# Kernel optimization log

Measured on AMD Instinct MI355X. Metric: run time of the kernel, lower is better.

Reference implementation:

```python
import jax, jax.numpy as jnp
import numpy as np

TEMPERATURE = 0.5
NEG_INF = -1e30  # mask value for diagonal in logsumexp (exact -inf also fine)


def _l2norm(x, eps=1e-12):
    # matches F.normalize(dim=1)
    n = jnp.sqrt(jnp.sum(x * x, axis=1, keepdims=True))
    return x / jnp.maximum(n, eps)


def setup_inputs() -> dict:
    key = jax.random.key(0)
    k1, k2, k3 = jax.random.split(key, 3)
    B, D, Q = 2048, 512, 32768
    return {
        "z_i": jax.random.normal(k1, (B, D), dtype=jnp.float32),
        "z_j": jax.random.normal(k2, (B, D), dtype=jnp.float32),
        "queue": jax.random.normal(k3, (Q, D), dtype=jnp.float32),
    }


def reference(z_i, z_j, queue):
    z = jnp.concatenate([z_i, z_j], axis=0)          # [N, D]
    N = z.shape[0]
    features = _l2norm(z)                            # [N, D]
    queue_norm = _l2norm(queue)                      # [Q, D]

    # NN retrieval from the support set
    sims_q = jnp.matmul(features, queue_norm.T)      # [N, Q]
    nn_idx = jnp.argmax(sims_q, axis=1)              # [N]
    nn_feats = queue_norm[nn_idx]                    # [N, D]

    # contrastive similarity between NNs and features
    sim = jnp.matmul(nn_feats, features.T) / TEMPERATURE  # [N, N]

    # positives: off-diagonals at +/- N//2
    sim_i_j = jnp.diagonal(sim, offset=N // 2)       # [N/2]
    sim_j_i = jnp.diagonal(sim, offset=-(N // 2))    # [N/2]
    positive_samples = jnp.concatenate([sim_i_j, sim_j_i], axis=0)  # [N]

    # negatives: all off-diagonal entries per row -> logsumexp with diag masked
    diag_mask = jnp.eye(N, dtype=bool)
    sim_masked = jnp.where(diag_mask, NEG_INF, sim)
    repulsion = jnp.mean(jax.scipy.special.logsumexp(sim_masked, axis=1))

    attraction = -jnp.mean(positive_samples)
    return attraction + repulsion
```

## Files before the change

### kernel.cpp

```cpp
#include <hip/hip_runtime.h>
#include <cstdint>

#define NFEAT 4096
#define NHALF 2048
#define DDIM  512
#define QROWS 32768

typedef unsigned short u16;
typedef unsigned char  u8;
typedef unsigned int   u32;
typedef unsigned long long u64;

typedef float  f32x16_t __attribute__((ext_vector_type(16)));
typedef int    i32x4_t  __attribute__((ext_vector_type(4)));
typedef int    i32x8_t  __attribute__((ext_vector_type(8)));

typedef const __attribute__((address_space(1))) void* gas_ptr;
typedef __attribute__((address_space(3))) void* las_ptr;

__device__ __forceinline__ u32 fkey(float f) {
  u32 u = __float_as_uint(f);
  return (u & 0x80000000u) ? ~u : (u | 0x80000000u);
}

__global__ void k_norm(const float* __restrict__ zi, const float* __restrict__ zj,
                       const float* __restrict__ queue,
                       u8* __restrict__ feat8T, u8* __restrict__ queue8T) {
  int gw = (int)((blockIdx.x * blockDim.x + threadIdx.x) >> 6);
  int lane = threadIdx.x & 63;
  const float* src; u8* dstT; int r31;
  if (gw < NFEAT) {
    src = (gw < NHALF) ? (zi + (size_t)gw * DDIM) : (zj + (size_t)(gw - NHALF) * DDIM);
    dstT = feat8T + (size_t)(gw >> 5) * 16384; r31 = gw & 31;
  } else {
    int r = gw - NFEAT;
    src = queue + (size_t)r * DDIM;
    dstT = queue8T + (size_t)(r >> 5) * 16384; r31 = r & 31;
  }
  float4 v0 = reinterpret_cast<const float4*>(src)[lane * 2];
  float4 v1 = reinterpret_cast<const float4*>(src)[lane * 2 + 1];
  float ss = v0.x*v0.x + v0.y*v0.y + v0.z*v0.z + v0.w*v0.w
           + v1.x*v1.x + v1.y*v1.y + v1.z*v1.z + v1.w*v1.w;
  #pragma unroll
  for (int off = 32; off >= 1; off >>= 1) ss += __shfl_xor(ss, off);
  float inv = 1.0f / fmaxf(sqrtf(ss), 1e-12f);
  float n0 = v0.x*inv, n1 = v0.y*inv, n2 = v0.z*inv, n3 = v0.w*inv;
  float n4 = v1.x*inv, n5 = v1.y*inv, n6 = v1.z*inv, n7 = v1.w*inv;
  u32 p01, p23, p45, p67;
  asm("v_cvt_pk_fp8_f32 %0, %1, %2" : "=v"(p01) : "v"(n0), "v"(n1));
  asm("v_cvt_pk_fp8_f32 %0, %1, %2" : "=v"(p23) : "v"(n2), "v"(n3));
  asm("v_cvt_pk_fp8_f32 %0, %1, %2" : "=v"(p45) : "v"(n4), "v"(n5));
  asm("v_cvt_pk_fp8_f32 %0, %1, %2" : "=v"(p67) : "v"(n6), "v"(n7));
  uint2 w8;
  w8.x = (p01 & 0xFFFFu) | (p23 << 16);
  w8.y = (p45 & 0xFFFFu) | (p67 << 16);
  size_t toff = (size_t)(lane >> 3) * 2048 + ((lane >> 2) & 1) * 1024
              + ((lane >> 1) & 1) * 512 + r31 * 16 + (lane & 1) * 8;
  *reinterpret_cast<uint2*>(dstT + toff) = w8;
}

#define SB0() __builtin_amdgcn_sched_barrier(0)
#define LGKM0_SB() do { asm volatile("s_waitcnt lgkmcnt(0)" ::: "memory"); SB0(); } while (0)
#define VMCNT4() asm volatile("s_waitcnt vmcnt(4)" ::: "memory")
#define VMCNT0() asm volatile("s_waitcnt vmcnt(0)" ::: "memory")
#define SBAR() __builtin_amdgcn_s_barrier()
#define RD(dst, base, off) asm volatile("ds_read_b128 %0, %1 offset:" off \
                                        : "=v"(dst) : "v"(base))
#define MFMA8(ACC, AV, BV) \
  ACC = __builtin_amdgcn_mfma_scale_f32_32x32x64_f8f6f4(AV, BV, ACC, 0, 0, 0, \
        0x7F7F7F7F, 0, 0x7F7F7F7F)

__global__ __launch_bounds__(512, 3) void k_argmax_gemm8(
    const u8* __restrict__ feat8T, const u8* __restrict__ queue8T,
    u64* __restrict__ part) {
  __shared__ u8 lds[16384];
  const int tid = threadIdx.x;
  const int w = tid >> 6, lane = tid & 63;
  const int wr = w >> 2, wc = w & 3;
  const int l31 = lane & 31, hi = lane >> 5;
  const int bid = (int)blockIdx.x;
  const int wg = (bid & 7) * 512 + (bid >> 3);
  const int mt = wg >> 4, ft = wg & 15;
  const int brow = mt * 128, bcol = ft * 256;

  const u8* pA = queue8T + (size_t)((brow >> 5) + (tid >> 7)) * 16384 + (tid & 127) * 16;
  const u32 dA = (u32)(size_t)(las_ptr)&lds[tid * 16];

  const u32 aAd = (u32)(size_t)(las_ptr)&lds[wr * 4096 + hi * 1024 + l31 * 16];

  const u8* pB0 = feat8T + (size_t)((bcol >> 5) + wc * 2) * 16384 + hi * 1024 + l31 * 16;
  const u8* pB1 = pB0 + 16384;

  f32x16_t acc00 = {}, acc01 = {}, acc10 = {}, acc11 = {};

  auto stageA = [&](int b, int t) {
    __builtin_amdgcn_global_load_lds((gas_ptr)(pA + t * 2048),
        (las_ptr)(size_t)(dA + (u32)(b * 8192)), 16, 0, 0);
  };

  stageA(0, 0);
  VMCNT0();
  SBAR();

  #pragma unroll
  for (int t = 0; t < 8; t++) {
    const u8* q0 = pB0 + t * 2048;
    const u8* q1 = pB1 + t * 2048;
    i32x4_t b0l = *reinterpret_cast<const i32x4_t*>(q0);
    i32x4_t b0h = *reinterpret_cast<const i32x4_t*>(q0 + 512);
    i32x4_t b1l = *reinterpret_cast<const i32x4_t*>(q1);
    i32x4_t b1h = *reinterpret_cast<const i32x4_t*>(q1 + 512);
    if (t < 7) stageA((t + 1) & 1, t + 1);
    const u32 xa = aAd + (u32)((t & 1) * 8192);
    i32x4_t a0l, a0h, a1l, a1h;
    RD(a0l, xa, "0");    RD(a0h, xa, "512");
    RD(a1l, xa, "2048"); RD(a1h, xa, "2560");
    LGKM0_SB();
    i32x8_t A0 = __builtin_shufflevector(a0l, a0h, 0, 1, 2, 3, 4, 5, 6, 7);
    i32x8_t A1 = __builtin_shufflevector(a1l, a1h, 0, 1, 2, 3, 4, 5, 6, 7);
    i32x8_t B0 = __builtin_shufflevector(b0l, b0h, 0, 1, 2, 3, 4, 5, 6, 7);
    i32x8_t B1 = __builtin_shufflevector(b1l, b1h, 0, 1, 2, 3, 4, 5, 6, 7);
    __builtin_amdgcn_s_setprio(1);
    MFMA8(acc00, A0, B0); MFMA8(acc01, A0, B1);
    MFMA8(acc10, A1, B0); MFMA8(acc11, A1, B1);
    __builtin_amdgcn_s_setprio(0);
    if (t < 7) { VMCNT0(); SBAR(); }
  }

  const int mslot = mt * 2 + wr;
#define AMAX_N(ACC0, ACC1, NOFF) do { \
    float bv = -3.0e38f; int br = 0; \
    _Pragma("unroll") \
    for (int reg = 0; reg < 16; reg++) { \
      float v = ACC0[reg]; int lr = (reg & 3) + 8 * (reg >> 2); \
      if (v > bv) { bv = v; br = lr; } } \
    _Pragma("unroll") \
    for (int reg = 0; reg < 16; reg++) { \
      float v = ACC1[reg]; int lr = 32 + (reg & 3) + 8 * (reg >> 2); \
      if (v > bv) { bv = v; br = lr; } } \
    u32 q = (u32)(brow + wr * 64 + br + 4 * hi); \
    u64 key = ((u64)fkey(bv) << 32) | (u64)(0xFFFFFFFFu - q); \
    u64 o = __shfl_xor(key, 32); \
    key = key > o ? key : o; \
    int j = bcol + wc * 64 + NOFF + l31; \
    if (hi == 0) part[(size_t)j * 512 + mslot] = key; \
  } while (0)
  AMAX_N(acc00, acc10, 0);
  AMAX_N(acc01, acc11, 32);
#undef AMAX_N
}

__global__ void k_reduce_gather(const u64* __restrict__ part,
                                const u8* __restrict__ queue8T,
                                u8* __restrict__ nn8T) {
  int row = (int)((blockIdx.x * blockDim.x + threadIdx.x) >> 6);
  int lane = threadIdx.x & 63;
  const u64* p = part + (size_t)row * 512;
  u64 best = 0;
  #pragma unroll
  for (int i = 0; i < 8; i++) { u64 v = p[lane * 8 + i]; best = best > v ? best : v; }
  #pragma unroll
  for (int off = 1; off < 64; off <<= 1) { u64 o = __shfl_xor(best, off); best = best > o ? best : o; }
  int g = (int)(0xFFFFFFFFu - (u32)(best & 0xFFFFFFFFu));
  if (lane < 32) {
    const uint4 v = *reinterpret_cast<const uint4*>(
        queue8T + (size_t)(g >> 5) * 16384 + lane * 512 + (g & 31) * 16);
    *reinterpret_cast<uint4*>(
        nn8T + (size_t)(row >> 5) * 16384 + lane * 512 + (row & 31) * 16) = v;
  }
}

#define FP8_TILE(XA, XB) do { \
    i32x4_t a00, a01, a10, a11, b00, b01, b10, b11; \
    RD(a00, XA, "0"); RD(a01, XA, "512"); \
    RD(a10, XA, "2048"); RD(a11, XA, "2560"); \
    RD(b00, XB, "0"); RD(b01, XB, "512"); \
    RD(b10, XB, "2048"); RD(b11, XB, "2560"); \
    LGKM0_SB(); \
    i32x8_t A0 = __builtin_shufflevector(a00, a01, 0, 1, 2, 3, 4, 5, 6, 7); \
    i32x8_t A1 = __builtin_shufflevector(a10, a11, 0, 1, 2, 3, 4, 5, 6, 7); \
    i32x8_t B0 = __builtin_shufflevector(b00, b01, 0, 1, 2, 3, 4, 5, 6, 7); \
    i32x8_t B1 = __builtin_shufflevector(b10, b11, 0, 1, 2, 3, 4, 5, 6, 7); \
    __builtin_amdgcn_s_setprio(1); \
    MFMA8(acc00, A0, B0); \
    MFMA8(acc01, A0, B1); \
    MFMA8(acc10, A1, B0); \
    MFMA8(acc11, A1, B1); \
    __builtin_amdgcn_s_setprio(0); \
  } while (0)

#define FP8_MAIN_LOOP() do { \
  stage(0, 0); stage(1, 1); \
  VMCNT4(); \
  SBAR(); \
  _Pragma("unroll") \
  for (int t = 0; t < 8; t++) { \
    if (t <= 5) stage((t + 2) % 3, t + 2); \
    const u32 bb = (u32)((t % 3) * 16384); \
    FP8_TILE(aAd + bb, bAd + bb); \
    if (t < 7) { \
      if (t <= 5) VMCNT4(); else VMCNT0(); \
      SBAR(); \
    } \
  } } while (0)

__global__ __launch_bounds__(256, 2) void k_sim_gemm8(
    const u8* __restrict__ feat8T, const u8* __restrict__ nn8T,
    float2* __restrict__ lsep, float* __restrict__ pos) {
  __shared__ u8 lds[49152];
  const int tid = threadIdx.x;
  const int w = tid >> 6, lane = tid & 63;
  const int wr = w >> 1, wc = w & 1;
  const int l31 = lane & 31, hi = lane >> 5;
  const int bid = (int)blockIdx.x;
  const int wg = (bid & 7) * 128 + (bid >> 3);
  const int mt = wg >> 5, nt = wg & 31;
  const int mtb = mt * 128, ntb = nt * 128;

  const u8* pA = feat8T + (size_t)(mtb >> 5) * 16384 + (tid >> 7) * 16384 + (tid & 127) * 16;
  const u8* pB = nn8T   + (size_t)(ntb >> 5) * 16384 + (tid >> 7) * 16384 + (tid & 127) * 16;
  const u32 dA = (u32)(size_t)(las_ptr)&lds[tid * 16];
  const u32 dB = dA + 8192;

  const u32 aAd = (u32)(size_t)(las_ptr)&lds[wr * 4096 + hi * 1024 + l31 * 16];
  const u32 bAd = (u32)(size_t)(las_ptr)&lds[8192 + wc * 4096 + hi * 1024 + l31 * 16];

  f32x16_t acc00 = {}, acc01 = {}, acc10 = {}, acc11 = {};

  auto stage = [&](int b, int t) {
    const u32 base = (u32)(b * 16384);
    __builtin_amdgcn_global_load_lds((gas_ptr)(pA + t * 2048),         (las_ptr)(size_t)(dA + base), 16, 0, 0);
    __builtin_amdgcn_global_load_lds((gas_ptr)(pA + 32768 + t * 2048), (las_ptr)(size_t)(dA + base + 4096), 16, 0, 0);
    __builtin_amdgcn_global_load_lds((gas_ptr)(pB + t * 2048),         (las_ptr)(size_t)(dB + base), 16, 0, 0);
    __builtin_amdgcn_global_load_lds((gas_ptr)(pB + 32768 + t * 2048), (las_ptr)(size_t)(dB + base + 4096), 16, 0, 0);
  };

  FP8_MAIN_LOOP();

  const int mslot = mt * 2 + wr;
  const int ibase = mtb + wr * 64 + 4 * hi;
  #pragma unroll
  for (int n = 0; n < 2; n++) {
    const int j = ntb + wc * 64 + n * 32 + l31;
    const int jp = j ^ NHALF;
    float mx = -3.0e38f;
    #pragma unroll
    for (int m = 0; m < 2; m++) {
      #pragma unroll
      for (int reg = 0; reg < 16; reg++) {
        float v = (n == 0 ? (m == 0 ? acc00[reg] : acc10[reg])
                          : (m == 0 ? acc01[reg] : acc11[reg])) * 2.0f;
        int i = ibase + m * 32 + (reg & 3) + 8 * (reg >> 2);
        if (i == jp) pos[j] = v;
        if (i == j) v = -1.0e30f;
        mx = fmaxf(mx, v);
      }
    }
    float sm = 0.f;
    #pragma unroll
    for (int m = 0; m < 2; m++) {
      #pragma unroll
      for (int reg = 0; reg < 16; reg++) {
        float v = (n == 0 ? (m == 0 ? acc00[reg] : acc10[reg])
                          : (m == 0 ? acc01[reg] : acc11[reg])) * 2.0f;
        int i = ibase + m * 32 + (reg & 3) + 8 * (reg >> 2);
        if (i == j) v = -1.0e30f;
        sm += __expf(v - mx);
      }
    }
    float mo = __shfl_xor(mx, 32);
    float so = __shfl_xor(sm, 32);
    float M = fmaxf(mx, mo);
    sm = sm * __expf(mx - M) + so * __expf(mo - M);
    if (hi == 0) lsep[(size_t)j * 64 + mslot] = make_float2(M, sm);
  }
}

__global__ void k_lse(const float2* __restrict__ lsep, float* __restrict__ lse) {
  int row = (int)((blockIdx.x * blockDim.x + threadIdx.x) >> 6);
  int lane = threadIdx.x & 63;
  float2 p = lsep[(size_t)row * 64 + lane];
  float m = p.x, s = p.y;
  #pragma unroll
  for (int off = 1; off < 64; off <<= 1) {
    float mo = __shfl_xor(m, off), so = __shfl_xor(s, off);
    float M = fmaxf(m, mo);
    s = s * __expf(m - M) + so * __expf(mo - M);
    m = M;
  }
  if (lane == 0) lse[row] = m + __logf(s);
}

__global__ void k_final(const float* __restrict__ lse, const float* __restrict__ pos,
                        float* __restrict__ out) {
  __shared__ float red[4];
  int tid = threadIdx.x;
  float a = 0.f;
  for (int i = tid; i < NFEAT; i += 256) a += lse[i] - pos[i];
  #pragma unroll
  for (int off = 32; off >= 1; off >>= 1) a += __shfl_xor(a, off);
  if ((tid & 63) == 0) red[tid >> 6] = a;
  __syncthreads();
  if (tid == 0) out[0] = (red[0] + red[1] + red[2] + red[3]) / (float)NFEAT;
}

extern "C" void kernel_launch(void* const* d_in, const int* in_sizes, int n_in,
                              void* d_out, int out_size, void* d_ws, size_t ws_size,
                              hipStream_t stream) {
  const float* zi    = (const float*)d_in[0];
  const float* zj    = (const float*)d_in[1];
  const float* queue = (const float*)d_in[2];
  float* out = (float*)d_out;
  char* ws = (char*)d_ws;

  u8*     queue8T = (u8*)(ws + 0);
  u8*     feat8T  = (u8*)(ws + 16777216);
  u8*     nn8T    = (u8*)(ws + 18874368);
  u64*    part    = (u64*)(ws + 20971520);
  float2* lsep    = (float2*)(ws + 37748736);
  float*  pos     = (float*)(ws + 39845888);
  float*  lse     = (float*)(ws + 39862272);

  k_norm<<<9216, 256, 0, stream>>>(zi, zj, queue, feat8T, queue8T);
  k_argmax_gemm8<<<4096, 512, 0, stream>>>(feat8T, queue8T, part);
  k_reduce_gather<<<1024, 256, 0, stream>>>(part, queue8T, nn8T);
  k_sim_gemm8<<<1024, 256, 0, stream>>>(feat8T, nn8T, lsep, pos);
  k_lse<<<1024, 256, 0, stream>>>(lsep, lse);
  k_final<<<1, 256, 0, stream>>>(lse, pos, out);
}
```

Baseline: 109.4 us.

## Halve waves per block, give each wave 64x128 tile, triple-buffer A staging

The argmax GEMM drops from 8 waves to 4 waves per 128x256 block, so each wave computes eight 32x32 MFMA accumulators instead of four. This reuses each A fragment read from LDS across four B tiles. The A staging moves from a double buffer to a triple buffer with waits of vmcnt(2), prefetching two K-steps ahead to overlap global-to-LDS loads with compute. The cost is more registers per wave (launch bounds 256,2), more LDS, and fewer waves to hide B global-load latency.

Result: slower. 115.9 us (+5.9%).

```diff
diff --git a/kernel.cpp b/kernel.cpp
--- a/kernel.cpp
+++ b/kernel.cpp
@@ -62,6 +62,7 @@
 #define SB0() __builtin_amdgcn_sched_barrier(0)
 #define LGKM0_SB() do { asm volatile("s_waitcnt lgkmcnt(0)" ::: "memory"); SB0(); } while (0)
 #define VMCNT4() asm volatile("s_waitcnt vmcnt(4)" ::: "memory")
+#define VMCNT2() asm volatile("s_waitcnt vmcnt(2)" ::: "memory")
 #define VMCNT0() asm volatile("s_waitcnt vmcnt(0)" ::: "memory")
 #define SBAR() __builtin_amdgcn_s_barrier()
 #define RD(dst, base, off) asm volatile("ds_read_b128 %0, %1 offset:" off \
@@ -70,13 +71,13 @@
   ACC = __builtin_amdgcn_mfma_scale_f32_32x32x64_f8f6f4(AV, BV, ACC, 0, 0, 0, \
         0x7F7F7F7F, 0, 0x7F7F7F7F)
 
-__global__ __launch_bounds__(512, 3) void k_argmax_gemm8(
+__global__ __launch_bounds__(256, 2) void k_argmax_gemm8(
     const u8* __restrict__ feat8T, const u8* __restrict__ queue8T,
     u64* __restrict__ part) {
-  __shared__ u8 lds[16384];
+  __shared__ u8 lds[24576];
   const int tid = threadIdx.x;
   const int w = tid >> 6, lane = tid & 63;
-  const int wr = w >> 2, wc = w & 3;
+  const int wr = w >> 1, wc = w & 1;
   const int l31 = lane & 31, hi = lane >> 5;
   const int bid = (int)blockIdx.x;
   const int wg = (bid & 7) * 512 + (bid >> 3);
@@ -88,43 +89,64 @@
 
   const u32 aAd = (u32)(size_t)(las_ptr)&lds[wr * 4096 + hi * 1024 + l31 * 16];
 
-  const u8* pB0 = feat8T + (size_t)((bcol >> 5) + wc * 2) * 16384 + hi * 1024 + l31 * 16;
+  const int lo = hi * 1024 + l31 * 16;
+  const u8* pB0 = feat8T + (size_t)((bcol >> 5) + wc * 4) * 16384 + lo;
   const u8* pB1 = pB0 + 16384;
-
-  f32x16_t acc00 = {}, acc01 = {}, acc10 = {}, acc11 = {};
+  const u8* pB2 = pB0 + 32768;
+  const u8* pB3 = pB0 + 49152;
+
+  f32x16_t acc00 = {}, acc01 = {}, acc02 = {}, acc03 = {};
+  f32x16_t acc10 = {}, acc11 = {}, acc12 = {}, acc13 = {};
 
   auto stageA = [&](int b, int t) {
+    const u32 base = (u32)(b * 8192);
     __builtin_amdgcn_global_load_lds((gas_ptr)(pA + t * 2048),
-        (las_ptr)(size_t)(dA + (u32)(b * 8192)), 16, 0, 0);
+        (las_ptr)(size_t)(dA + base), 16, 0, 0);
+    __builtin_amdgcn_global_load_lds((gas_ptr)(pA + 32768 + t * 2048),
+        (las_ptr)(size_t)(dA + base + 4096), 16, 0, 0);
   };
 
-  stageA(0, 0);
-  VMCNT0();
+  stageA(0, 0); stageA(1, 1);
+  VMCNT2();
   SBAR();
 
   #pragma unroll
   for (int t = 0; t < 8; t++) {
+    if (t <= 5) stageA((t + 2) % 3, t + 2);
     const u8* q0 = pB0 + t * 2048;
     const u8* q1 = pB1 + t * 2048;
+    const u8* q2 = pB2 + t * 2048;
+    const u8* q3 = pB3 + t * 2048;
     i32x4_t b0l = *reinterpret_cast<const i32x4_t*>(q0);
     i32x4_t b0h = *reinterpret_cast<const i32x4_t*>(q0 + 512);
     i32x4_t b1l = *reinterpret_cast<const i32x4_t*>(q1);
     i32x4_t b1h = *reinterpret_cast<const i32x4_t*>(q1 + 512);
-    if (t < 7) stageA((t + 1) & 1, t + 1);
-    const u32 xa = aAd + (u32)((t & 1) * 8192);
-    i32x4_t a0l, a0h, a1l, a1h;
-    RD(a0l, xa, "0");    RD(a0h, xa, "512");
-    RD(a1l, xa, "2048"); RD(a1h, xa, "2560");
+    i32x4_t b2l = *reinterpret_cast<const i32x4_t*>(q2);
+    i32x4_t b2h = *reinterpret_cast<const i32x4_t*>(q2 + 512);
+    i32x4_t b3l = *reinterpret_cast<const i32x4_t*>(q3);
+    i32x4_t b3h = *reinterpret_cast<const i32x4_t*>(q3 + 512);
+    const u32 xa = aAd + (u32)((t % 3) * 8192);
+    i32x4_t r0, r1, r2, r3;
+    RD(r0, xa, "0");    RD(r1, xa, "512");
+    RD(r2, xa, "2048"); RD(r3, xa, "2560");
     LGKM0_SB();
-    i32x8_t A0 = __builtin_shufflevector(a0l, a0h, 0, 1, 2, 3, 4, 5, 6, 7);
-    i32x8_t A1 = __builtin_shufflevector(a1l, a1h, 0, 1, 2, 3, 4, 5, 6, 7);
+    i32x8_t A0 = __builtin_shufflevector(r0, r1, 0, 1, 2, 3, 4, 5, 6, 7);
+    i32x8_t A1 = __builtin_shufflevector(r2, r3, 0, 1, 2, 3, 4, 5, 6, 7);
     i32x8_t B0 = __builtin_shufflevector(b0l, b0h, 0, 1, 2, 3, 4, 5, 6, 7);
     i32x8_t B1 = __builtin_shufflevector(b1l, b1h, 0, 1, 2, 3, 4, 5, 6, 7);
+    i32x8_t B2 = __builtin_shufflevector(b2l, b2h, 0, 1, 2, 3, 4, 5, 6, 7);
+    i32x8_t B3 = __builtin_shufflevector(b3l, b3h, 0, 1, 2, 3, 4, 5, 6, 7);
     __builtin_amdgcn_s_setprio(1);
     MFMA8(acc00, A0, B0); MFMA8(acc01, A0, B1);
+    MFMA8(acc02, A0, B2); MFMA8(acc03, A0, B3);
     MFMA8(acc10, A1, B0); MFMA8(acc11, A1, B1);
+    MFMA8(acc12, A1, B2); MFMA8(acc13, A1, B3);
     __builtin_amdgcn_s_setprio(0);
-    if (t < 7) { VMCNT0(); SBAR(); }
+    if (t < 7) {
+      SB0();
+      if (t <= 5) VMCNT2(); else VMCNT0();
+      SBAR();
+    }
   }
 
   const int mslot = mt * 2 + wr;
@@ -142,11 +164,13 @@
     u64 key = ((u64)fkey(bv) << 32) | (u64)(0xFFFFFFFFu - q); \
     u64 o = __shfl_xor(key, 32); \
     key = key > o ? key : o; \
-    int j = bcol + wc * 64 + NOFF + l31; \
+    int j = bcol + wc * 128 + NOFF + l31; \
     if (hi == 0) part[(size_t)j * 512 + mslot] = key; \
   } while (0)
   AMAX_N(acc00, acc10, 0);
   AMAX_N(acc01, acc11, 32);
+  AMAX_N(acc02, acc12, 64);
+  AMAX_N(acc03, acc13, 96);
 #undef AMAX_N
 }
 
@@ -322,7 +346,7 @@
   float*  lse     = (float*)(ws + 39862272);
 
   k_norm<<<9216, 256, 0, stream>>>(zi, zj, queue, feat8T, queue8T);
-  k_argmax_gemm8<<<4096, 512, 0, stream>>>(feat8T, queue8T, part);
+  k_argmax_gemm8<<<4096, 256, 0, stream>>>(feat8T, queue8T, part);
   k_reduce_gather<<<1024, 256, 0, stream>>>(part, queue8T, nn8T);
   k_sim_gemm8<<<1024, 256, 0, stream>>>(feat8T, nn8T, lsep, pos);
   k_lse<<<1024, 256, 0, stream>>>(lsep, lse);
```
